# Kernel optimization log

Measured on AMD Instinct MI355X. Metric: run time of the kernel, lower is better.

Reference implementation:

```python
import jax, jax.numpy as jnp
import numpy as np

L = 15          # mp_iterations
D = 128         # node/edge feature dim
N = 50000       # n_nodes
E = 800000      # n_edges
EPS = 1e-5      # LayerNorm eps


def _mlp_ln(h, W1, b1, W2, b2, W3, b3, g, beta):
    """Linear->ReLU->Linear->ReLU->Linear->LayerNorm (torch defaults)."""
    h = jax.nn.relu(h @ W1 + b1)
    h = jax.nn.relu(h @ W2 + b2)
    h = h @ W3 + b3
    mu = h.mean(-1, keepdims=True)
    var = ((h - mu) ** 2).mean(-1, keepdims=True)
    return (h - mu) * jax.lax.rsqrt(var + EPS) * g + beta


def setup_inputs() -> dict:
    key = jax.random.key(0)
    ks = jax.random.split(key, 12)
    scale = 0.05
    x = jax.random.normal(ks[0], (N, D), dtype=jnp.float32)
    edge_index = jax.random.randint(ks[1], (2, E), 0, N, dtype=jnp.int64)
    edge_attr = jax.random.normal(ks[2], (E, D), dtype=jnp.float32)
    # Per-block stacked params (leading dim L) for edge MLP (in=3D) and node MLP (in=2D).
    inp = {
        "x": x, "edge_index": edge_index, "edge_attr": edge_attr,
        "eW1": jax.random.normal(ks[3], (L, 3 * D, D), jnp.float32) * scale,
        "eb1": jnp.zeros((L, D), jnp.float32),
        "eW2": jax.random.normal(ks[4], (L, D, D), jnp.float32) * scale,
        "eb2": jnp.zeros((L, D), jnp.float32),
        "eW3": jax.random.normal(ks[5], (L, D, D), jnp.float32) * scale,
        "eb3": jnp.zeros((L, D), jnp.float32),
        "eg": jnp.ones((L, D), jnp.float32),
        "ebeta": jnp.zeros((L, D), jnp.float32),
        "nW1": jax.random.normal(ks[6], (L, 2 * D, D), jnp.float32) * scale,
        "nb1": jnp.zeros((L, D), jnp.float32),
        "nW2": jax.random.normal(ks[7], (L, D, D), jnp.float32) * scale,
        "nb2": jnp.zeros((L, D), jnp.float32),
        "nW3": jax.random.normal(ks[8], (L, D, D), jnp.float32) * scale,
        "nb3": jnp.zeros((L, D), jnp.float32),
        "ng": jnp.ones((L, D), jnp.float32),
        "nbeta": jnp.zeros((L, D), jnp.float32),
    }
    return inp


def reference(x, edge_index, edge_attr,
              eW1, eb1, eW2, eb2, eW3, eb3, eg, ebeta,
              nW1, nb1, nW2, nb2, nW3, nb3, ng, nbeta):
    row, col = edge_index[0], edge_index[1]
    n_nodes = x.shape[0]

    params = dict(eW1=eW1, eb1=eb1, eW2=eW2, eb2=eb2, eW3=eW3, eb3=eb3,
                  eg=eg, ebeta=ebeta,
                  nW1=nW1, nb1=nb1, nW2=nW2, nb2=nb2, nW3=nW3, nb3=nb3,
                  ng=ng, nbeta=nbeta)

    def block(carry, p):
        xc, ea = carry
        # Edge update: concat(src, dest, edge_attr) -> MLP -> residual
        m = jnp.concatenate([xc[row], xc[col], ea], axis=-1)      # [E, 3D]
        ea = ea + _mlp_ln(m, p["eW1"], p["eb1"], p["eW2"], p["eb2"],
                          p["eW3"], p["eb3"], p["eg"], p["ebeta"])
        # Node update: scatter_sum over destination, concat -> MLP -> residual
        agg = jax.ops.segment_sum(ea, col, num_segments=n_nodes)  # [N, D]
        h = jnp.concatenate([xc, agg], axis=-1)                    # [N, 2D]
        xc = xc + _mlp_ln(h, p["nW1"], p["nb1"], p["nW2"], p["nb2"],
                          p["nW3"], p["nb3"], p["ng"], p["nbeta"])
        return (xc, ea), None

    (x, edge_attr), _ = jax.lax.scan(block, (x, edge_attr), params)
    return x, edge_attr
```

## Files before the change

kernel.cpp:

```cpp
#include <hip/hip_runtime.h>
#include <hip/hip_bf16.h>

#define L_ITERS 15
#define DD 128
#define NNODES 50000
#define NEDGES 800000

typedef __attribute__((ext_vector_type(4))) float f32x4;
typedef __attribute__((ext_vector_type(8))) short bf16x8;

static __device__ __forceinline__ unsigned short f2bf(float f) {
  union { float f; unsigned u; } v; v.f = f;
  unsigned r = v.u + 0x7FFFu + ((v.u >> 16) & 1u);
  return (unsigned short)(r >> 16);
}
static __device__ __forceinline__ float bf2f(unsigned short h) {
  union { unsigned u; float f; } v; v.u = (unsigned)h << 16; return v.f;
}

__global__ void pack_w_kernel(const float* __restrict__ src,
                              unsigned short* __restrict__ dst, int K) {
  int total = L_ITERS * K * DD;
  for (int i = blockIdx.x * blockDim.x + threadIdx.x; i < total;
       i += gridDim.x * blockDim.x) {
    int layer = i / (K * DD);
    int rem = i - layer * K * DD;
    int k = rem / DD, n = rem - (rem / DD) * DD;
    int s = k >> 5, hi = (k >> 3) & 3, j = k & 7;
    int t = n >> 4, lane = hi * 16 + (n & 15);
    dst[layer * K * DD + ((s * 8 + t) * 64 + lane) * 8 + j] = f2bf(src[i]);
  }
}

__global__ void cvt_kernel(const float* __restrict__ src,
                           unsigned short* __restrict__ dst,
                           int nrows, int dstride) {
  int total = nrows * 16;
  for (int p = blockIdx.x * blockDim.x + threadIdx.x; p < total;
       p += gridDim.x * blockDim.x) {
    int r = p >> 4, w = p & 15;
    const float* s = src + (long long)r * DD + w * 8;
    f32x4 a = *(const f32x4*)s, b = *(const f32x4*)(s + 4);
    bf16x8 o;
    o[0] = (short)f2bf(a[0]); o[1] = (short)f2bf(a[1]);
    o[2] = (short)f2bf(a[2]); o[3] = (short)f2bf(a[3]);
    o[4] = (short)f2bf(b[0]); o[5] = (short)f2bf(b[1]);
    o[6] = (short)f2bf(b[2]); o[7] = (short)f2bf(b[3]);
    *(bf16x8*)(dst + (long long)r * dstride + w * 8) = o;
  }
}

__global__ void hist_kernel(const int* __restrict__ ei, int* __restrict__ cnt) {
  for (int e = blockIdx.x * blockDim.x + threadIdx.x; e < NEDGES;
       e += gridDim.x * blockDim.x)
    atomicAdd(&cnt[ei[NEDGES + e]], 1);
}

__global__ __launch_bounds__(1024) void scan_kernel(const int* __restrict__ cnt,
                                                    int* __restrict__ off,
                                                    int* __restrict__ cursor) {
  __shared__ int buf[1024];
  __shared__ int base;
  if (threadIdx.x == 0) { base = 0; off[0] = 0; }
  __syncthreads();
  for (int start = 0; start < NNODES; start += 1024) {
    int i = start + threadIdx.x;
    int v = (i < NNODES) ? cnt[i] : 0;
    buf[threadIdx.x] = v;
    __syncthreads();
    for (int d = 1; d < 1024; d <<= 1) {
      int t = (threadIdx.x >= d) ? buf[threadIdx.x - d] : 0;
      __syncthreads();
      buf[threadIdx.x] += t;
      __syncthreads();
    }
    if (i < NNODES) {
      int incl = base + buf[threadIdx.x];
      off[i + 1] = incl;
      cursor[i] = incl - v;
    }
    __syncthreads();
    if (threadIdx.x == 0) base += buf[1023];
    __syncthreads();
  }
}

__global__ void scatter_kernel(const int* __restrict__ ei, int* __restrict__ cursor,
                               int* __restrict__ perm) {
  for (int e = blockIdx.x * blockDim.x + threadIdx.x; e < NEDGES;
       e += gridDim.x * blockDim.x) {
    int p = atomicAdd(&cursor[ei[NEDGES + e]], 1);
    perm[p] = e;
  }
}

template <int NS, int ROWS, int MI>
static __device__ __forceinline__ void gemm_step(
    const unsigned short* A, const unsigned short* __restrict__ pw,
    const float* __restrict__ bias, f32x4 (&acc)[MI][2],
    int lrow, int lhi, int lane, int wv, int wcol0) {
  float bv0 = bias[wcol0 + lrow];
  float bv1 = bias[wcol0 + 16 + lrow];
#pragma unroll
  for (int mi = 0; mi < MI; ++mi) {
    f32x4 z0, z1;
    z0[0] = bv0; z0[1] = bv0; z0[2] = bv0; z0[3] = bv0;
    z1[0] = bv1; z1[1] = bv1; z1[2] = bv1; z1[3] = bv1;
    acc[mi][0] = z0; acc[mi][1] = z1;
  }
  const unsigned short* bp = pw + (wv * 2 * 64 + lane) * 8;
#pragma unroll
  for (int s = 0; s < NS; ++s) {
    bf16x8 w0 = *(const bf16x8*)(bp + s * 4096);
    bf16x8 w1 = *(const bf16x8*)(bp + s * 4096 + 512);
    const unsigned short* ap = A + (s >> 2) * (ROWS * 136) + (s & 3) * 32 + lhi * 8;
#pragma unroll
    for (int mi = 0; mi < MI; ++mi) {
      bf16x8 a = *(const bf16x8*)(ap + (mi * 16 + lrow) * 136);
      acc[mi][0] = __builtin_amdgcn_mfma_f32_16x16x32_bf16(a, w0, acc[mi][0], 0, 0, 0);
      acc[mi][1] = __builtin_amdgcn_mfma_f32_16x16x32_bf16(a, w1, acc[mi][1], 0, 0, 0);
    }
  }
}

template <int MI>
static __device__ __forceinline__ void relu_store(const f32x4 (&acc)[MI][2],
                                                  unsigned short* H,
                                                  int lrow, int lhi, int wcol0) {
#pragma unroll
  for (int mi = 0; mi < MI; ++mi)
#pragma unroll
    for (int ni = 0; ni < 2; ++ni)
#pragma unroll
      for (int j = 0; j < 4; ++j)
        H[(mi * 16 + lhi * 4 + j) * 136 + wcol0 + ni * 16 + lrow] =
            f2bf(fmaxf(acc[mi][ni][j], 0.f));
}

template <bool LAST>
__global__ __launch_bounds__(256) void edge_kernel(
    const unsigned short* __restrict__ xbf, unsigned short* easlot,
    const int* __restrict__ ei,
    const unsigned short* __restrict__ pw1,
    const unsigned short* __restrict__ pw2,
    const unsigned short* __restrict__ pw3,
    const float* __restrict__ b1, const float* __restrict__ b2,
    const float* __restrict__ b3, const float* __restrict__ gg,
    const float* __restrict__ bb) {
  __shared__ unsigned short sm[3 * 64 * 136];
  __shared__ float red[128];
  constexpr int PL = 64 * 136;
  const int tid = threadIdx.x, lane = tid & 63, wv = tid >> 6;
  const int lrow = lane & 15, lhi = lane >> 4, wcol0 = wv * 32;
  const int block0 = blockIdx.x * 64;

  if (tid < 128) red[tid] = 0.f;

  {
    int r = tid >> 2, q = tid & 3;
    long long e = block0 + r;
    const unsigned short* s0 = xbf + (long long)ei[e] * DD;
    const unsigned short* s1 = xbf + (long long)ei[NEDGES + e] * DD;
    const unsigned short* s2 = easlot + e * 256;
#pragma unroll
    for (int k = 0; k < 12; ++k) {
      int w = q + 4 * k;
      int plane = w >> 4, off = (w & 15) * 8;
      const unsigned short* sp = (plane == 0) ? s0 : (plane == 1 ? s1 : s2);
      *(bf16x8*)(&sm[plane * PL + r * 136 + off]) = *(const bf16x8*)(sp + off);
    }
  }
  __syncthreads();

  f32x4 acc[4][2];
  gemm_step<12, 64, 4>(sm, pw1, b1, acc, lrow, lhi, lane, wv, wcol0);
  __syncthreads();
  relu_store<4>(acc, sm, lrow, lhi, wcol0);
  __syncthreads();
  gemm_step<4, 64, 4>(sm, pw2, b2, acc, lrow, lhi, lane, wv, wcol0);
  relu_store<4>(acc, sm + PL, lrow, lhi, wcol0);
  __syncthreads();
  gemm_step<4, 64, 4>(sm + PL, pw3, b3, acc, lrow, lhi, lane, wv, wcol0);

  float ps[4][4], pq[4][4];
#pragma unroll
  for (int mi = 0; mi < 4; ++mi)
#pragma unroll
    for (int j = 0; j < 4; ++j) {
      float a = acc[mi][0][j], b = acc[mi][1][j];
      ps[mi][j] = a + b;
      pq[mi][j] = a * a + b * b;
    }
#pragma unroll
  for (int m = 1; m < 16; m <<= 1)
#pragma unroll
    for (int mi = 0; mi < 4; ++mi)
#pragma unroll
      for (int j = 0; j < 4; ++j) {
        ps[mi][j] += __shfl_xor(ps[mi][j], m);
        pq[mi][j] += __shfl_xor(pq[mi][j], m);
      }
  if (lrow == 0)
#pragma unroll
    for (int mi = 0; mi < 4; ++mi)
#pragma unroll
      for (int j = 0; j < 4; ++j) {
        int rl = mi * 16 + lhi * 4 + j;
        atomicAdd(&red[rl * 2], ps[mi][j]);
        atomicAdd(&red[rl * 2 + 1], pq[mi][j]);
      }
  __syncthreads();

  float gv[2], bv[2];
  gv[0] = gg[wcol0 + lrow]; gv[1] = gg[wcol0 + 16 + lrow];
  bv[0] = bb[wcol0 + lrow]; bv[1] = bb[wcol0 + 16 + lrow];
  const unsigned short* P2 = sm + 2 * PL;
  float* eaf = (float*)easlot;
#pragma unroll
  for (int mi = 0; mi < 4; ++mi)
#pragma unroll
    for (int j = 0; j < 4; ++j) {
      int rl = mi * 16 + lhi * 4 + j;
      long long e = block0 + rl;
      float mu = red[rl * 2] * (1.f / DD);
      float var = red[rl * 2 + 1] * (1.f / DD) - mu * mu;
      float rstd = rsqrtf(var + 1e-5f);
#pragma unroll
      for (int ni = 0; ni < 2; ++ni) {
        int c = wcol0 + ni * 16 + lrow;
        float nv = bf2f(P2[rl * 136 + c]) +
                   (acc[mi][ni][j] - mu) * rstd * gv[ni] + bv[ni];
        if (LAST) eaf[e * 128 + c] = nv;
        else sm[rl * 136 + c] = f2bf(nv);
      }
    }
  if (!LAST) {
    __syncthreads();
#pragma unroll
    for (int p = tid; p < 1024; p += 256) {
      int r = p >> 4, off = (p & 15) * 8;
      *(bf16x8*)(easlot + (long long)(block0 + r) * 256 + off) =
          *(const bf16x8*)(sm + r * 136 + off);
    }
  }
}

template <bool LAST>
__global__ __launch_bounds__(256) void node_kernel(
    unsigned short* xbf, const unsigned short* __restrict__ easlot,
    float* xout,
    const int* __restrict__ off, const int* __restrict__ perm,
    const unsigned short* __restrict__ pw1,
    const unsigned short* __restrict__ pw2,
    const unsigned short* __restrict__ pw3,
    const float* __restrict__ b1, const float* __restrict__ b2,
    const float* __restrict__ b3, const float* __restrict__ gg,
    const float* __restrict__ bb) {
  __shared__ unsigned short sm[2 * 32 * 136];
  __shared__ float red[64];
  constexpr int PL = 32 * 136;
  const int tid = threadIdx.x, lane = tid & 63, wv = tid >> 6;
  const int lrow = lane & 15, lhi = lane >> 4, wcol0 = wv * 32;
  const int block0 = blockIdx.x * 32;

  if (tid < 64) red[tid] = 0.f;

  {
    int r = tid >> 3, c8 = tid & 7;
    int grow = block0 + r;
    int gr = grow < NNODES ? grow : NNODES - 1;
    const unsigned short* xs = xbf + (long long)gr * DD + c8 * 16;
    *(bf16x8*)(&sm[r * 136 + c8 * 16]) = *(const bf16x8*)xs;
    *(bf16x8*)(&sm[r * 136 + c8 * 16 + 8]) = *(const bf16x8*)(xs + 8);
    float a[16];
#pragma unroll
    for (int i = 0; i < 16; ++i) a[i] = 0.f;
    int p0 = off[gr], p1 = off[gr + 1];
    if (!LAST) {
      for (int p = p0; p < p1; ++p) {
        const unsigned short* ep = easlot + (long long)perm[p] * 256 + c8 * 16;
        bf16x8 u = *(const bf16x8*)ep;
        bf16x8 v = *(const bf16x8*)(ep + 8);
#pragma unroll
        for (int i = 0; i < 8; ++i) {
          a[i] += bf2f((unsigned short)u[i]);
          a[8 + i] += bf2f((unsigned short)v[i]);
        }
      }
    } else {
      const float* eaf = (const float*)easlot;
      for (int p = p0; p < p1; ++p) {
        const float* ep = eaf + (long long)perm[p] * 128 + c8 * 16;
        f32x4 u0 = *(const f32x4*)ep, u1 = *(const f32x4*)(ep + 4);
        f32x4 u2 = *(const f32x4*)(ep + 8), u3 = *(const f32x4*)(ep + 12);
#pragma unroll
        for (int i = 0; i < 4; ++i) {
          a[i] += u0[i]; a[4 + i] += u1[i]; a[8 + i] += u2[i]; a[12 + i] += u3[i];
        }
      }
    }
    bf16x8 o0, o1;
#pragma unroll
    for (int i = 0; i < 8; ++i) {
      o0[i] = (short)f2bf(a[i]);
      o1[i] = (short)f2bf(a[8 + i]);
    }
    *(bf16x8*)(&sm[PL + r * 136 + c8 * 16]) = o0;
    *(bf16x8*)(&sm[PL + r * 136 + c8 * 16 + 8]) = o1;
  }
  __syncthreads();

  f32x4 acc[2][2];
  gemm_step<8, 32, 2>(sm, pw1, b1, acc, lrow, lhi, lane, wv, wcol0);
  __syncthreads();
  relu_store<2>(acc, sm, lrow, lhi, wcol0);
  __syncthreads();
  gemm_step<4, 32, 2>(sm, pw2, b2, acc, lrow, lhi, lane, wv, wcol0);
  relu_store<2>(acc, sm + PL, lrow, lhi, wcol0);
  __syncthreads();
  gemm_step<4, 32, 2>(sm + PL, pw3, b3, acc, lrow, lhi, lane, wv, wcol0);

  float ps[2][4], pq[2][4];
#pragma unroll
  for (int mi = 0; mi < 2; ++mi)
#pragma unroll
    for (int j = 0; j < 4; ++j) {
      float a = acc[mi][0][j], b = acc[mi][1][j];
      ps[mi][j] = a + b;
      pq[mi][j] = a * a + b * b;
    }
#pragma unroll
  for (int m = 1; m < 16; m <<= 1)
#pragma unroll
    for (int mi = 0; mi < 2; ++mi)
#pragma unroll
      for (int j = 0; j < 4; ++j) {
        ps[mi][j] += __shfl_xor(ps[mi][j], m);
        pq[mi][j] += __shfl_xor(pq[mi][j], m);
      }
  if (lrow == 0)
#pragma unroll
    for (int mi = 0; mi < 2; ++mi)
#pragma unroll
      for (int j = 0; j < 4; ++j) {
        int rl = mi * 16 + lhi * 4 + j;
        atomicAdd(&red[rl * 2], ps[mi][j]);
        atomicAdd(&red[rl * 2 + 1], pq[mi][j]);
      }
  __syncthreads();

  float gv[2], bv[2];
  gv[0] = gg[wcol0 + lrow]; gv[1] = gg[wcol0 + 16 + lrow];
  bv[0] = bb[wcol0 + lrow]; bv[1] = bb[wcol0 + 16 + lrow];
#pragma unroll
  for (int mi = 0; mi < 2; ++mi)
#pragma unroll
    for (int j = 0; j < 4; ++j) {
      int rl = mi * 16 + lhi * 4 + j;
      int grow = block0 + rl;
      if (grow < NNODES) {
        float mu = red[rl * 2] * (1.f / DD);
        float var = red[rl * 2 + 1] * (1.f / DD) - mu * mu;
        float rstd = rsqrtf(var + 1e-5f);
#pragma unroll
        for (int ni = 0; ni < 2; ++ni) {
          int c = wcol0 + ni * 16 + lrow;
          float nv = bf2f(xbf[(long long)grow * DD + c]) +
                     (acc[mi][ni][j] - mu) * rstd * gv[ni] + bv[ni];
          if (LAST) xout[(long long)grow * DD + c] = nv;
          else sm[rl * 136 + c] = f2bf(nv);
        }
      }
    }
  if (!LAST) {
    __syncthreads();
#pragma unroll
    for (int p = tid; p < 512; p += 256) {
      int r = p >> 4, off2 = (p & 15) * 8;
      int grow = block0 + r;
      if (grow < NNODES)
        *(bf16x8*)(xbf + (long long)grow * DD + off2) =
            *(const bf16x8*)(sm + r * 136 + off2);
    }
  }
}

extern "C" void kernel_launch(void* const* d_in, const int* in_sizes, int n_in,
                              void* d_out, int out_size, void* d_ws, size_t ws_size,
                              hipStream_t stream) {
  const float* x  = (const float*)d_in[0];
  const int* ei   = (const int*)d_in[1];
  const float* ea = (const float*)d_in[2];
  const float* eW1 = (const float*)d_in[3];
  const float* eb1 = (const float*)d_in[4];
  const float* eW2 = (const float*)d_in[5];
  const float* eb2 = (const float*)d_in[6];
  const float* eW3 = (const float*)d_in[7];
  const float* eb3 = (const float*)d_in[8];
  const float* eg  = (const float*)d_in[9];
  const float* ebt = (const float*)d_in[10];
  const float* nW1 = (const float*)d_in[11];
  const float* nb1 = (const float*)d_in[12];
  const float* nW2 = (const float*)d_in[13];
  const float* nb2 = (const float*)d_in[14];
  const float* nW3 = (const float*)d_in[15];
  const float* nb3 = (const float*)d_in[16];
  const float* ng  = (const float*)d_in[17];
  const float* nbt = (const float*)d_in[18];

  float* xout = (float*)d_out;
  unsigned short* easlot =
      (unsigned short*)(xout + (size_t)NNODES * DD);

  unsigned short* pk_eW1 = (unsigned short*)d_ws;
  unsigned short* pk_eW2 = pk_eW1 + (size_t)L_ITERS * 384 * DD;
  unsigned short* pk_eW3 = pk_eW2 + (size_t)L_ITERS * DD * DD;
  unsigned short* pk_nW1 = pk_eW3 + (size_t)L_ITERS * DD * DD;
  unsigned short* pk_nW2 = pk_nW1 + (size_t)L_ITERS * 256 * DD;
  unsigned short* pk_nW3 = pk_nW2 + (size_t)L_ITERS * DD * DD;
  unsigned short* xbf = pk_nW3 + (size_t)L_ITERS * DD * DD;
  int* cursor = (int*)(xbf + (size_t)NNODES * DD);
  int* off    = cursor + NNODES;
  int* perm   = off + NNODES + 1;
  size_t need = (size_t)((char*)(perm + NEDGES) - (char*)d_ws);
  if (ws_size < need) return;

  pack_w_kernel<<<1024, 256, 0, stream>>>(eW1, pk_eW1, 384);
  pack_w_kernel<<<1024, 256, 0, stream>>>(eW2, pk_eW2, 128);
  pack_w_kernel<<<1024, 256, 0, stream>>>(eW3, pk_eW3, 128);
  pack_w_kernel<<<1024, 256, 0, stream>>>(nW1, pk_nW1, 256);
  pack_w_kernel<<<1024, 256, 0, stream>>>(nW2, pk_nW2, 128);
  pack_w_kernel<<<1024, 256, 0, stream>>>(nW3, pk_nW3, 128);

  cvt_kernel<<<1024, 256, 0, stream>>>(x, xbf, NNODES, 128);
  cvt_kernel<<<4096, 256, 0, stream>>>(ea, easlot, NEDGES, 256);

  hipMemsetAsync(cursor, 0, NNODES * sizeof(int), stream);
  hist_kernel<<<2048, 256, 0, stream>>>(ei, cursor);
  scan_kernel<<<1, 1024, 0, stream>>>(cursor, off, cursor);
  scatter_kernel<<<2048, 256, 0, stream>>>(ei, cursor, perm);

  for (int l = 0; l < L_ITERS; ++l) {
    if (l < L_ITERS - 1) {
      edge_kernel<false><<<NEDGES / 64, 256, 0, stream>>>(
          xbf, easlot, ei,
          pk_eW1 + (size_t)l * 384 * DD, pk_eW2 + (size_t)l * DD * DD,
          pk_eW3 + (size_t)l * DD * DD,
          eb1 + l * DD, eb2 + l * DD, eb3 + l * DD, eg + l * DD, ebt + l * DD);
      node_kernel<false><<<(NNODES + 31) / 32, 256, 0, stream>>>(
          xbf, easlot, xout, off, perm,
          pk_nW1 + (size_t)l * 256 * DD, pk_nW2 + (size_t)l * DD * DD,
          pk_nW3 + (size_t)l * DD * DD,
          nb1 + l * DD, nb2 + l * DD, nb3 + l * DD, ng + l * DD, nbt + l * DD);
    } else {
      edge_kernel<true><<<NEDGES / 64, 256, 0, stream>>>(
          xbf, easlot, ei,
          pk_eW1 + (size_t)l * 384 * DD, pk_eW2 + (size_t)l * DD * DD,
          pk_eW3 + (size_t)l * DD * DD,
          eb1 + l * DD, eb2 + l * DD, eb3 + l * DD, eg + l * DD, ebt + l * DD);
      node_kernel<true><<<(NNODES + 31) / 32, 256, 0, stream>>>(
          xbf, easlot, xout, off, perm,
          pk_nW1 + (size_t)l * 256 * DD, pk_nW2 + (size_t)l * DD * DD,
          pk_nW3 + (size_t)l * DD * DD,
          nb1 + l * DD, nb2 + l * DD, nb3 + l * DD, ng + l * DD, nbt + l * DD);
    }
  }
}
```

Before: 5.186 ms.

## Swizzle shared-memory tiles and restructure LayerNorm epilogue as row-wise vectorized pass

```diff
diff --git a/kernel.cpp b/kernel.cpp
--- a/kernel.cpp
+++ b/kernel.cpp
@@ -109,14 +109,16 @@
     acc[mi][0] = z0; acc[mi][1] = z1;
   }
   const unsigned short* bp = pw + (wv * 2 * 64 + lane) * 8;
+  const int swz = (lrow & 7) << 3;
 #pragma unroll
   for (int s = 0; s < NS; ++s) {
     bf16x8 w0 = *(const bf16x8*)(bp + s * 4096);
     bf16x8 w1 = *(const bf16x8*)(bp + s * 4096 + 512);
-    const unsigned short* ap = A + (s >> 2) * (ROWS * 136) + (s & 3) * 32 + lhi * 8;
+    const unsigned short* ap =
+        A + (s >> 2) * (ROWS * 128) + (((s & 3) * 32 + lhi * 8) ^ swz);
 #pragma unroll
     for (int mi = 0; mi < MI; ++mi) {
-      bf16x8 a = *(const bf16x8*)(ap + (mi * 16 + lrow) * 136);
+      bf16x8 a = *(const bf16x8*)(ap + (mi * 16 + lrow) * 128);
       acc[mi][0] = __builtin_amdgcn_mfma_f32_16x16x32_bf16(a, w0, acc[mi][0], 0, 0, 0);
       acc[mi][1] = __builtin_amdgcn_mfma_f32_16x16x32_bf16(a, w1, acc[mi][1], 0, 0, 0);
     }
@@ -130,11 +132,30 @@
 #pragma unroll
   for (int mi = 0; mi < MI; ++mi)
 #pragma unroll
-    for (int ni = 0; ni < 2; ++ni)
-#pragma unroll
-      for (int j = 0; j < 4; ++j)
-        H[(mi * 16 + lhi * 4 + j) * 136 + wcol0 + ni * 16 + lrow] =
+    for (int j = 0; j < 4; ++j) {
+      int row = mi * 16 + lhi * 4 + j;
+      int sw = (row & 7) << 3;
+#pragma unroll
+      for (int ni = 0; ni < 2; ++ni)
+        H[row * 128 + ((wcol0 + ni * 16 + lrow) ^ sw)] =
             f2bf(fmaxf(acc[mi][ni][j], 0.f));
+    }
+}
+
+template <int MI>
+static __device__ __forceinline__ void acc_store(const f32x4 (&acc)[MI][2],
+                                                 float* F,
+                                                 int lrow, int lhi, int wcol0) {
+#pragma unroll
+  for (int mi = 0; mi < MI; ++mi)
+#pragma unroll
+    for (int j = 0; j < 4; ++j) {
+      int row = mi * 16 + lhi * 4 + j;
+      int sw = (row & 7) << 2;
+#pragma unroll
+      for (int ni = 0; ni < 2; ++ni)
+        F[row * 128 + ((wcol0 + ni * 16 + lrow) ^ sw)] = acc[mi][ni][j];
+    }
 }
 
 template <bool LAST>
@@ -147,9 +168,9 @@
     const float* __restrict__ b1, const float* __restrict__ b2,
     const float* __restrict__ b3, const float* __restrict__ gg,
     const float* __restrict__ bb) {
-  __shared__ unsigned short sm[3 * 64 * 136];
+  constexpr int PL = 64 * 128;
+  __shared__ unsigned short sm[3 * PL];
   __shared__ float red[128];
-  constexpr int PL = 64 * 136;
   const int tid = threadIdx.x, lane = tid & 63, wv = tid >> 6;
   const int lrow = lane & 15, lhi = lane >> 4, wcol0 = wv * 32;
   const int block0 = blockIdx.x * 64;
@@ -162,12 +183,13 @@
     const unsigned short* s0 = xbf + (long long)ei[e] * DD;
     const unsigned short* s1 = xbf + (long long)ei[NEDGES + e] * DD;
     const unsigned short* s2 = easlot + e * 256;
+    const int sw = (r & 7) << 3;
 #pragma unroll
     for (int k = 0; k < 12; ++k) {
       int w = q + 4 * k;
       int plane = w >> 4, off = (w & 15) * 8;
       const unsigned short* sp = (plane == 0) ? s0 : (plane == 1 ? s1 : s2);
-      *(bf16x8*)(&sm[plane * PL + r * 136 + off]) = *(const bf16x8*)(sp + off);
+      *(bf16x8*)(&sm[plane * PL + r * 128 + (off ^ sw)]) = *(const bf16x8*)(sp + off);
     }
   }
   __syncthreads();
@@ -181,66 +203,57 @@
   relu_store<4>(acc, sm + PL, lrow, lhi, wcol0);
   __syncthreads();
   gemm_step<4, 64, 4>(sm + PL, pw3, b3, acc, lrow, lhi, lane, wv, wcol0);
-
-  float ps[4][4], pq[4][4];
-#pragma unroll
-  for (int mi = 0; mi < 4; ++mi)
-#pragma unroll
-    for (int j = 0; j < 4; ++j) {
-      float a = acc[mi][0][j], b = acc[mi][1][j];
-      ps[mi][j] = a + b;
-      pq[mi][j] = a * a + b * b;
-    }
-#pragma unroll
-  for (int m = 1; m < 16; m <<= 1)
-#pragma unroll
-    for (int mi = 0; mi < 4; ++mi)
-#pragma unroll
-      for (int j = 0; j < 4; ++j) {
-        ps[mi][j] += __shfl_xor(ps[mi][j], m);
-        pq[mi][j] += __shfl_xor(pq[mi][j], m);
-      }
-  if (lrow == 0)
-#pragma unroll
-    for (int mi = 0; mi < 4; ++mi)
-#pragma unroll
-      for (int j = 0; j < 4; ++j) {
-        int rl = mi * 16 + lhi * 4 + j;
-        atomicAdd(&red[rl * 2], ps[mi][j]);
-        atomicAdd(&red[rl * 2 + 1], pq[mi][j]);
-      }
-  __syncthreads();
-
-  float gv[2], bv[2];
-  gv[0] = gg[wcol0 + lrow]; gv[1] = gg[wcol0 + 16 + lrow];
-  bv[0] = bb[wcol0 + lrow]; bv[1] = bb[wcol0 + 16 + lrow];
+  __syncthreads();
+
+  float* F = (float*)sm;
+  acc_store<4>(acc, F, lrow, lhi, wcol0);
+  __syncthreads();
+
+  const int row = tid >> 2, cg = tid & 3;
+  const int fsw = (row & 7) << 2;
+  f32x4 av[8];
+  float s = 0.f, q2 = 0.f;
+#pragma unroll
+  for (int k = 0; k < 8; ++k) {
+    av[k] = *(const f32x4*)(F + row * 128 + ((cg * 32 + k * 4) ^ fsw));
+#pragma unroll
+    for (int i = 0; i < 4; ++i) { s += av[k][i]; q2 += av[k][i] * av[k][i]; }
+  }
+  atomicAdd(&red[row * 2], s);
+  atomicAdd(&red[row * 2 + 1], q2);
+  __syncthreads();
+
+  float mu = red[row * 2] * (1.f / DD);
+  float var = red[row * 2 + 1] * (1.f / DD) - mu * mu;
+  float rstd = rsqrtf(var + 1e-5f);
   const unsigned short* P2 = sm + 2 * PL;
+  const int ssw = (row & 7) << 3;
+  long long e = block0 + row;
   float* eaf = (float*)easlot;
 #pragma unroll
-  for (int mi = 0; mi < 4; ++mi)
-#pragma unroll
-    for (int j = 0; j < 4; ++j) {
-      int rl = mi * 16 + lhi * 4 + j;
-      long long e = block0 + rl;
-      float mu = red[rl * 2] * (1.f / DD);
-      float var = red[rl * 2 + 1] * (1.f / DD) - mu * mu;
-      float rstd = rsqrtf(var + 1e-5f);
-#pragma unroll
-      for (int ni = 0; ni < 2; ++ni) {
-        int c = wcol0 + ni * 16 + lrow;
-        float nv = bf2f(P2[rl * 136 + c]) +
-                   (acc[mi][ni][j] - mu) * rstd * gv[ni] + bv[ni];
-        if (LAST) eaf[e * 128 + c] = nv;
-        else sm[rl * 136 + c] = f2bf(nv);
-      }
-    }
-  if (!LAST) {
-    __syncthreads();
-#pragma unroll
-    for (int p = tid; p < 1024; p += 256) {
-      int r = p >> 4, off = (p & 15) * 8;
-      *(bf16x8*)(easlot + (long long)(block0 + r) * 256 + off) =
-          *(const bf16x8*)(sm + r * 136 + off);
+  for (int k = 0; k < 4; ++k) {
+    int c0 = cg * 32 + k * 8;
+    bf16x8 rv = *(const bf16x8*)(P2 + row * 128 + (c0 ^ ssw));
+    f32x4 g0 = *(const f32x4*)(gg + c0), g1 = *(const f32x4*)(gg + c0 + 4);
+    f32x4 t0 = *(const f32x4*)(bb + c0), t1 = *(const f32x4*)(bb + c0 + 4);
+    f32x4 lo = av[2 * k], hi = av[2 * k + 1];
+    float nv[8];
+#pragma unroll
+    for (int i = 0; i < 4; ++i) {
+      nv[i]     = bf2f((unsigned short)rv[i])     + (lo[i] - mu) * rstd * g0[i] + t0[i];
+      nv[4 + i] = bf2f((unsigned short)rv[4 + i]) + (hi[i] - mu) * rstd * g1[i] + t1[i];
+    }
+    if (LAST) {
+      f32x4 o0, o1;
+#pragma unroll
+      for (int i = 0; i < 4; ++i) { o0[i] = nv[i]; o1[i] = nv[4 + i]; }
+      *(f32x4*)(eaf + e * 128 + c0) = o0;
+      *(f32x4*)(eaf + e * 128 + c0 + 4) = o1;
+    } else {
+      bf16x8 o;
+#pragma unroll
+      for (int i = 0; i < 8; ++i) o[i] = (short)f2bf(nv[i]);
+      *(bf16x8*)(easlot + e * 256 + c0) = o;
     }
   }
 }
@@ -256,9 +269,10 @@
     const float* __restrict__ b1, const float* __restrict__ b2,
     const float* __restrict__ b3, const float* __restrict__ gg,
     const float* __restrict__ bb) {
-  __shared__ unsigned short sm[2 * 32 * 136];
+  constexpr int PL = 32 * 128;
+  __shared__ unsigned short sm[2 * PL];
+  __shared__ float Fbuf[32 * 128];
   __shared__ float red[64];
-  constexpr int PL = 32 * 136;
   const int tid = threadIdx.x, lane = tid & 63, wv = tid >> 6;
   const int lrow = lane & 15, lhi = lane >> 4, wcol0 = wv * 32;
   const int block0 = blockIdx.x * 32;
@@ -269,9 +283,10 @@
     int r = tid >> 3, c8 = tid & 7;
     int grow = block0 + r;
     int gr = grow < NNODES ? grow : NNODES - 1;
+    const int sw = (r & 7) << 3;
     const unsigned short* xs = xbf + (long long)gr * DD + c8 * 16;
-    *(bf16x8*)(&sm[r * 136 + c8 * 16]) = *(const bf16x8*)xs;
-    *(bf16x8*)(&sm[r * 136 + c8 * 16 + 8]) = *(const bf16x8*)(xs + 8);
+    *(bf16x8*)(&sm[r * 128 + ((c8 * 16) ^ sw)]) = *(const bf16x8*)xs;
+    *(bf16x8*)(&sm[r * 128 + ((c8 * 16 + 8) ^ sw)]) = *(const bf16x8*)(xs + 8);
     float a[16];
 #pragma unroll
     for (int i = 0; i < 16; ++i) a[i] = 0.f;
@@ -305,82 +320,70 @@
       o0[i] = (short)f2bf(a[i]);
       o1[i] = (short)f2bf(a[8 + i]);
     }
-    *(bf16x8*)(&sm[PL + r * 136 + c8 * 16]) = o0;
-    *(bf16x8*)(&sm[PL + r * 136 + c8 * 16 + 8]) = o1;
-  }
-  __syncthreads();
-
+    *(bf16x8*)(&sm[PL + r * 128 + ((c8 * 16) ^ sw)]) = o0;
+    *(bf16x8*)(&sm[PL + r * 128 + ((c8 * 16 + 8) ^ sw)]) = o1;
+  }
+  __syncthreads();
+
+  unsigned short* H1 = (unsigned short*)Fbuf;
+  unsigned short* H2 = H1 + PL;
   f32x4 acc[2][2];
   gemm_step<8, 32, 2>(sm, pw1, b1, acc, lrow, lhi, lane, wv, wcol0);
-  __syncthreads();
-  relu_store<2>(acc, sm, lrow, lhi, wcol0);
-  __syncthreads();
-  gemm_step<4, 32, 2>(sm, pw2, b2, acc, lrow, lhi, lane, wv, wcol0);
-  relu_store<2>(acc, sm + PL, lrow, lhi, wcol0);
-  __syncthreads();
-  gemm_step<4, 32, 2>(sm + PL, pw3, b3, acc, lrow, lhi, lane, wv, wcol0);
-
-  float ps[2][4], pq[2][4];
-#pragma unroll
-  for (int mi = 0; mi < 2; ++mi)
-#pragma unroll
-    for (int j = 0; j < 4; ++j) {
-      float a = acc[mi][0][j], b = acc[mi][1][j];
-      ps[mi][j] = a + b;
-      pq[mi][j] = a * a + b * b;
-    }
-#pragma unroll
-  for (int m = 1; m < 16; m <<= 1)
-#pragma unroll
-    for (int mi = 0; mi < 2; ++mi)
-#pragma unroll
-      for (int j = 0; j < 4; ++j) {
-        ps[mi][j] += __shfl_xor(ps[mi][j], m);
-        pq[mi][j] += __shfl_xor(pq[mi][j], m);
+  relu_store<2>(acc, H1, lrow, lhi, wcol0);
+  __syncthreads();
+  gemm_step<4, 32, 2>(H1, pw2, b2, acc, lrow, lhi, lane, wv, wcol0);
+  relu_store<2>(acc, H2, lrow, lhi, wcol0);
+  __syncthreads();
+  gemm_step<4, 32, 2>(H2, pw3, b3, acc, lrow, lhi, lane, wv, wcol0);
+  __syncthreads();
+  acc_store<2>(acc, Fbuf, lrow, lhi, wcol0);
+  __syncthreads();
+
+  const int row = tid >> 3, cg = tid & 7;
+  const int fsw = (row & 7) << 2;
+  f32x4 av[4];
+  float s = 0.f, q2 = 0.f;
+#pragma unroll
+  for (int k = 0; k < 4; ++k) {
+    av[k] = *(const f32x4*)(Fbuf + row * 128 + ((cg * 16 + k * 4) ^ fsw));
+#pragma unroll
+    for (int i = 0; i < 4; ++i) { s += av[k][i]; q2 += av[k][i] * av[k][i]; }
+  }
+  atomicAdd(&red[row * 2], s);
+  atomicAdd(&red[row * 2 + 1], q2);
+  __syncthreads();
+
+  int grow = block0 + row;
+  if (grow < NNODES) {
+    float mu = red[row * 2] * (1.f / DD);
+    float var = red[row * 2 + 1] * (1.f / DD) - mu * mu;
+    float rstd = rsqrtf(var + 1e-5f);
+    const int ssw = (row & 7) << 3;
+#pragma unroll
+    for (int k = 0; k < 2; ++k) {
+      int c0 = cg * 16 + k * 8;
+      bf16x8 rv = *(const bf16x8*)(sm + row * 128 + (c0 ^ ssw));
+      f32x4 g0 = *(const f32x4*)(gg + c0), g1 = *(const f32x4*)(gg + c0 + 4);
+      f32x4 t0 = *(const f32x4*)(bb + c0), t1 = *(const f32x4*)(bb + c0 + 4);
+      f32x4 lo = av[2 * k], hi = av[2 * k + 1];
+      float nv[8];
+#pragma unroll
+      for (int i = 0; i < 4; ++i) {
+        nv[i]     = bf2f((unsigned short)rv[i])     + (lo[i] - mu) * rstd * g0[i] + t0[i];
+        nv[4 + i] = bf2f((unsigned short)rv[4 + i]) + (hi[i] - mu) * rstd * g1[i] + t1[i];
       }
-  if (lrow == 0)
-#pragma unroll
-    for (int mi = 0; mi < 2; ++mi)
-#pragma unroll
-      for (int j = 0; j < 4; ++j) {
-        int rl = mi * 16 + lhi * 4 + j;
-        atomicAdd(&red[rl * 2], ps[mi][j]);
-        atomicAdd(&red[rl * 2 + 1], pq[mi][j]);
+      if (LAST) {
+        f32x4 o0, o1;
+#pragma unroll
+        for (int i = 0; i < 4; ++i) { o0[i] = nv[i]; o1[i] = nv[4 + i]; }
+        *(f32x4*)(xout + (long long)grow * DD + c0) = o0;
+        *(f32x4*)(xout + (long long)grow * DD + c0 + 4) = o1;
+      } else {
+        bf16x8 o;
+#pragma unroll
+        for (int i = 0; i < 8; ++i) o[i] = (short)f2bf(nv[i]);
+        *(bf16x8*)(xbf + (long long)grow * DD + c0) = o;
       }
-  __syncthreads();
-
-  float gv[2], bv[2];
-  gv[0] = gg[wcol0 + lrow]; gv[1] = gg[wcol0 + 16 + lrow];
-  bv[0] = bb[wcol0 + lrow]; bv[1] = bb[wcol0 + 16 + lrow];
-#pragma unroll
-  for (int mi = 0; mi < 2; ++mi)
-#pragma unroll
-    for (int j = 0; j < 4; ++j) {
-      int rl = mi * 16 + lhi * 4 + j;
-      int grow = block0 + rl;
-      if (grow < NNODES) {
-        float mu = red[rl * 2] * (1.f / DD);
-        float var = red[rl * 2 + 1] * (1.f / DD) - mu * mu;
-        float rstd = rsqrtf(var + 1e-5f);
-#pragma unroll
-        for (int ni = 0; ni < 2; ++ni) {
-          int c = wcol0 + ni * 16 + lrow;
-          float nv = bf2f(xbf[(long long)grow * DD + c]) +
-                     (acc[mi][ni][j] - mu) * rstd * gv[ni] + bv[ni];
-          if (LAST) xout[(long long)grow * DD + c] = nv;
-          else sm[rl * 136 + c] = f2bf(nv);
-        }
-      }
-    }
-  if (!LAST) {
-    __syncthreads();
-#pragma unroll
-    for (int p = tid; p < 512; p += 256) {
-      int r = p >> 4, off2 = (p & 15) * 8;
-      int grow = block0 + r;
-      if (grow < NNODES)
-        *(bf16x8*)(xbf + (long long)grow * DD + off2) =
-            *(const bf16x8*)(sm + r * 136 + off2);
     }
   }
 }
```

New measurement: 6.493 ms. +25.2%, slower.

## Shrink edge kernel LDS by reading edge_attr operand directly from global

Applied to the files above, without the earlier changes.

```diff
diff --git a/kernel.cpp b/kernel.cpp
--- a/kernel.cpp
+++ b/kernel.cpp
@@ -138,7 +138,7 @@
 }
 
 template <bool LAST>
-__global__ __launch_bounds__(256) void edge_kernel(
+__global__ __launch_bounds__(256, 4) void edge_kernel(
     const unsigned short* __restrict__ xbf, unsigned short* easlot,
     const int* __restrict__ ei,
     const unsigned short* __restrict__ pw1,
@@ -147,9 +147,9 @@
     const float* __restrict__ b1, const float* __restrict__ b2,
     const float* __restrict__ b3, const float* __restrict__ gg,
     const float* __restrict__ bb) {
-  __shared__ unsigned short sm[3 * 64 * 136];
+  constexpr int PL = 64 * 136;
+  __shared__ unsigned short sm[2 * PL];
   __shared__ float red[128];
-  constexpr int PL = 64 * 136;
   const int tid = threadIdx.x, lane = tid & 63, wv = tid >> 6;
   const int lrow = lane & 15, lhi = lane >> 4, wcol0 = wv * 32;
   const int block0 = blockIdx.x * 64;
@@ -161,19 +161,45 @@
     long long e = block0 + r;
     const unsigned short* s0 = xbf + (long long)ei[e] * DD;
     const unsigned short* s1 = xbf + (long long)ei[NEDGES + e] * DD;
-    const unsigned short* s2 = easlot + e * 256;
-#pragma unroll
-    for (int k = 0; k < 12; ++k) {
+#pragma unroll
+    for (int k = 0; k < 8; ++k) {
       int w = q + 4 * k;
       int plane = w >> 4, off = (w & 15) * 8;
-      const unsigned short* sp = (plane == 0) ? s0 : (plane == 1 ? s1 : s2);
+      const unsigned short* sp = (plane == 0) ? s0 : s1;
       *(bf16x8*)(&sm[plane * PL + r * 136 + off]) = *(const bf16x8*)(sp + off);
     }
   }
   __syncthreads();
 
   f32x4 acc[4][2];
-  gemm_step<12, 64, 4>(sm, pw1, b1, acc, lrow, lhi, lane, wv, wcol0);
+  {
+    float bv0 = b1[wcol0 + lrow], bv1 = b1[wcol0 + 16 + lrow];
+#pragma unroll
+    for (int mi = 0; mi < 4; ++mi) {
+      f32x4 z0, z1;
+      z0[0] = bv0; z0[1] = bv0; z0[2] = bv0; z0[3] = bv0;
+      z1[0] = bv1; z1[1] = bv1; z1[2] = bv1; z1[3] = bv1;
+      acc[mi][0] = z0; acc[mi][1] = z1;
+    }
+    const unsigned short* bp = pw1 + (wv * 2 * 64 + lane) * 8;
+#pragma unroll
+    for (int s = 0; s < 12; ++s) {
+      bf16x8 w0 = *(const bf16x8*)(bp + s * 4096);
+      bf16x8 w1 = *(const bf16x8*)(bp + s * 4096 + 512);
+#pragma unroll
+      for (int mi = 0; mi < 4; ++mi) {
+        bf16x8 a;
+        if (s < 8)
+          a = *(const bf16x8*)(sm + (s >> 2) * PL + (mi * 16 + lrow) * 136 +
+                               (s & 3) * 32 + lhi * 8);
+        else
+          a = *(const bf16x8*)(easlot + (long long)(block0 + mi * 16 + lrow) * 256 +
+                               (s - 8) * 32 + lhi * 8);
+        acc[mi][0] = __builtin_amdgcn_mfma_f32_16x16x32_bf16(a, w0, acc[mi][0], 0, 0, 0);
+        acc[mi][1] = __builtin_amdgcn_mfma_f32_16x16x32_bf16(a, w1, acc[mi][1], 0, 0, 0);
+      }
+    }
+  }
   __syncthreads();
   relu_store<4>(acc, sm, lrow, lhi, wcol0);
   __syncthreads();
@@ -214,8 +240,7 @@
   float gv[2], bv[2];
   gv[0] = gg[wcol0 + lrow]; gv[1] = gg[wcol0 + 16 + lrow];
   bv[0] = bb[wcol0 + lrow]; bv[1] = bb[wcol0 + 16 + lrow];
-  const unsigned short* P2 = sm + 2 * PL;
-  float* eaf = (float*)easlot;
+  float* F = (float*)sm;
 #pragma unroll
   for (int mi = 0; mi < 4; ++mi)
 #pragma unroll
@@ -228,19 +253,27 @@
 #pragma unroll
       for (int ni = 0; ni < 2; ++ni) {
         int c = wcol0 + ni * 16 + lrow;
-        float nv = bf2f(P2[rl * 136 + c]) +
+        float nv = bf2f(easlot[e * 256 + c]) +
                    (acc[mi][ni][j] - mu) * rstd * gv[ni] + bv[ni];
-        if (LAST) eaf[e * 128 + c] = nv;
+        if (LAST) F[rl * 128 + c] = nv;
         else sm[rl * 136 + c] = f2bf(nv);
       }
     }
-  if (!LAST) {
-    __syncthreads();
+  __syncthreads();
+  if (LAST) {
+    float* eaf = (float*)easlot;
+#pragma unroll
+    for (int p = tid; p < 2048; p += 256) {
+      int r = p >> 5, o = (p & 31) * 4;
+      *(f32x4*)(eaf + (long long)(block0 + r) * 128 + o) =
+          *(const f32x4*)(F + r * 128 + o);
+    }
+  } else {
 #pragma unroll
     for (int p = tid; p < 1024; p += 256) {
-      int r = p >> 4, off = (p & 15) * 8;
-      *(bf16x8*)(easlot + (long long)(block0 + r) * 256 + off) =
-          *(const bf16x8*)(sm + r * 136 + off);
+      int r = p >> 4, o = (p & 15) * 8;
+      *(bf16x8*)(easlot + (long long)(block0 + r) * 256 + o) =
+          *(const bf16x8*)(sm + r * 136 + o);
     }
   }
 }
```

Measured after the change: 6.359 ms. 1.23x slower.

## Give each wave its own 16-edge tile in edge MLP kernel, dropping block barriers

Applied to the files above, without the earlier changes.

```diff
diff --git a/kernel.cpp b/kernel.cpp
--- a/kernel.cpp
+++ b/kernel.cpp
@@ -138,7 +138,7 @@
 }
 
 template <bool LAST>
-__global__ __launch_bounds__(256) void edge_kernel(
+__global__ __launch_bounds__(256, 3) void edge_kernel(
     const unsigned short* __restrict__ xbf, unsigned short* easlot,
     const int* __restrict__ ei,
     const unsigned short* __restrict__ pw1,
@@ -147,100 +147,159 @@
     const float* __restrict__ b1, const float* __restrict__ b2,
     const float* __restrict__ b3, const float* __restrict__ gg,
     const float* __restrict__ bb) {
-  __shared__ unsigned short sm[3 * 64 * 136];
-  __shared__ float red[128];
-  constexpr int PL = 64 * 136;
+  __shared__ unsigned short sm[4 * 16 * 384];
   const int tid = threadIdx.x, lane = tid & 63, wv = tid >> 6;
-  const int lrow = lane & 15, lhi = lane >> 4, wcol0 = wv * 32;
-  const int block0 = blockIdx.x * 64;
-
-  if (tid < 128) red[tid] = 0.f;
+  const int lrow = lane & 15, lhi = lane >> 4;
+  unsigned short* R = sm + wv * (16 * 384);
+  const long long block0 = (long long)blockIdx.x * 64 + wv * 16;
 
   {
-    int r = tid >> 2, q = tid & 3;
+    int r = lane >> 2, q = lane & 3;
     long long e = block0 + r;
     const unsigned short* s0 = xbf + (long long)ei[e] * DD;
     const unsigned short* s1 = xbf + (long long)ei[NEDGES + e] * DD;
     const unsigned short* s2 = easlot + e * 256;
+    const int swz = (r & 7) << 3;
 #pragma unroll
     for (int k = 0; k < 12; ++k) {
       int w = q + 4 * k;
       int plane = w >> 4, off = (w & 15) * 8;
-      const unsigned short* sp = (plane == 0) ? s0 : (plane == 1 ? s1 : s2);
-      *(bf16x8*)(&sm[plane * PL + r * 136 + off]) = *(const bf16x8*)(sp + off);
-    }
-  }
-  __syncthreads();
-
-  f32x4 acc[4][2];
-  gemm_step<12, 64, 4>(sm, pw1, b1, acc, lrow, lhi, lane, wv, wcol0);
-  __syncthreads();
-  relu_store<4>(acc, sm, lrow, lhi, wcol0);
-  __syncthreads();
-  gemm_step<4, 64, 4>(sm, pw2, b2, acc, lrow, lhi, lane, wv, wcol0);
-  relu_store<4>(acc, sm + PL, lrow, lhi, wcol0);
-  __syncthreads();
-  gemm_step<4, 64, 4>(sm + PL, pw3, b3, acc, lrow, lhi, lane, wv, wcol0);
-
-  float ps[4][4], pq[4][4];
-#pragma unroll
-  for (int mi = 0; mi < 4; ++mi)
-#pragma unroll
-    for (int j = 0; j < 4; ++j) {
-      float a = acc[mi][0][j], b = acc[mi][1][j];
-      ps[mi][j] = a + b;
-      pq[mi][j] = a * a + b * b;
-    }
-#pragma unroll
-  for (int m = 1; m < 16; m <<= 1)
-#pragma unroll
-    for (int mi = 0; mi < 4; ++mi)
-#pragma unroll
-      for (int j = 0; j < 4; ++j) {
-        ps[mi][j] += __shfl_xor(ps[mi][j], m);
-        pq[mi][j] += __shfl_xor(pq[mi][j], m);
-      }
-  if (lrow == 0)
-#pragma unroll
-    for (int mi = 0; mi < 4; ++mi)
-#pragma unroll
-      for (int j = 0; j < 4; ++j) {
-        int rl = mi * 16 + lhi * 4 + j;
-        atomicAdd(&red[rl * 2], ps[mi][j]);
-        atomicAdd(&red[rl * 2 + 1], pq[mi][j]);
-      }
-  __syncthreads();
-
-  float gv[2], bv[2];
-  gv[0] = gg[wcol0 + lrow]; gv[1] = gg[wcol0 + 16 + lrow];
-  bv[0] = bb[wcol0 + lrow]; bv[1] = bb[wcol0 + 16 + lrow];
-  const unsigned short* P2 = sm + 2 * PL;
-  float* eaf = (float*)easlot;
-#pragma unroll
-  for (int mi = 0; mi < 4; ++mi)
-#pragma unroll
-    for (int j = 0; j < 4; ++j) {
-      int rl = mi * 16 + lhi * 4 + j;
-      long long e = block0 + rl;
-      float mu = red[rl * 2] * (1.f / DD);
-      float var = red[rl * 2 + 1] * (1.f / DD) - mu * mu;
-      float rstd = rsqrtf(var + 1e-5f);
-#pragma unroll
-      for (int ni = 0; ni < 2; ++ni) {
-        int c = wcol0 + ni * 16 + lrow;
-        float nv = bf2f(P2[rl * 136 + c]) +
-                   (acc[mi][ni][j] - mu) * rstd * gv[ni] + bv[ni];
-        if (LAST) eaf[e * 128 + c] = nv;
-        else sm[rl * 136 + c] = f2bf(nv);
-      }
-    }
-  if (!LAST) {
-    __syncthreads();
-#pragma unroll
-    for (int p = tid; p < 1024; p += 256) {
-      int r = p >> 4, off = (p & 15) * 8;
-      *(bf16x8*)(easlot + (long long)(block0 + r) * 256 + off) =
-          *(const bf16x8*)(sm + r * 136 + off);
+      const unsigned short* sp = plane == 0 ? s0 : (plane == 1 ? s1 : s2);
+      *(bf16x8*)(&R[r * 384 + plane * 128 + (off ^ swz)]) =
+          *(const bf16x8*)(sp + off);
+    }
+  }
+
+  const int aswz = (lrow & 7) << 3;
+  f32x4 acc[8];
+
+  {
+#pragma unroll
+    for (int t = 0; t < 8; ++t) {
+      float bv = b1[t * 16 + lrow];
+      f32x4 z; z[0] = bv; z[1] = bv; z[2] = bv; z[3] = bv;
+      acc[t] = z;
+    }
+#pragma unroll
+    for (int s = 0; s < 12; ++s) {
+      bf16x8 a = *(const bf16x8*)(
+          &R[lrow * 384 + (s >> 2) * 128 + ((((s & 3) * 32) + lhi * 8) ^ aswz)]);
+#pragma unroll
+      for (int t = 0; t < 8; ++t) {
+        bf16x8 w = *(const bf16x8*)(pw1 + ((s * 8 + t) * 64 + lane) * 8);
+        acc[t] = __builtin_amdgcn_mfma_f32_16x16x32_bf16(a, w, acc[t], 0, 0, 0);
+      }
+    }
+  }
+#pragma unroll
+  for (int j = 0; j < 4; ++j) {
+    int row = lhi * 4 + j;
+    int swz = (row & 7) << 3;
+#pragma unroll
+    for (int t = 0; t < 8; ++t)
+      R[row * 384 + ((t * 16 + lrow) ^ swz)] = f2bf(fmaxf(acc[t][j], 0.f));
+  }
+
+  {
+#pragma unroll
+    for (int t = 0; t < 8; ++t) {
+      float bv = b2[t * 16 + lrow];
+      f32x4 z; z[0] = bv; z[1] = bv; z[2] = bv; z[3] = bv;
+      acc[t] = z;
+    }
+#pragma unroll
+    for (int s = 0; s < 4; ++s) {
+      bf16x8 a = *(const bf16x8*)(&R[lrow * 384 + ((s * 32 + lhi * 8) ^ aswz)]);
+#pragma unroll
+      for (int t = 0; t < 8; ++t) {
+        bf16x8 w = *(const bf16x8*)(pw2 + ((s * 8 + t) * 64 + lane) * 8);
+        acc[t] = __builtin_amdgcn_mfma_f32_16x16x32_bf16(a, w, acc[t], 0, 0, 0);
+      }
+    }
+  }
+#pragma unroll
+  for (int j = 0; j < 4; ++j) {
+    int row = lhi * 4 + j;
+    int swz = (row & 7) << 3;
+#pragma unroll
+    for (int t = 0; t < 8; ++t)
+      R[row * 384 + 128 + ((t * 16 + lrow) ^ swz)] = f2bf(fmaxf(acc[t][j], 0.f));
+  }
+
+  {
+#pragma unroll
+    for (int t = 0; t < 8; ++t) {
+      float bv = b3[t * 16 + lrow];
+      f32x4 z; z[0] = bv; z[1] = bv; z[2] = bv; z[3] = bv;
+      acc[t] = z;
+    }
+#pragma unroll
+    for (int s = 0; s < 4; ++s) {
+      bf16x8 a = *(const bf16x8*)(
+          &R[lrow * 384 + 128 + ((s * 32 + lhi * 8) ^ aswz)]);
+#pragma unroll
+      for (int t = 0; t < 8; ++t) {
+        bf16x8 w = *(const bf16x8*)(pw3 + ((s * 8 + t) * 64 + lane) * 8);
+        acc[t] = __builtin_amdgcn_mfma_f32_16x16x32_bf16(a, w, acc[t], 0, 0, 0);
+      }
+    }
+  }
+
+  float mu[4], rstd[4];
+#pragma unroll
+  for (int j = 0; j < 4; ++j) {
+    float s = 0.f, q2 = 0.f;
+#pragma unroll
+    for (int t = 0; t < 8; ++t) { float v = acc[t][j]; s += v; q2 += v * v; }
+#pragma unroll
+    for (int m = 1; m < 16; m <<= 1) {
+      s += __shfl_xor(s, m);
+      q2 += __shfl_xor(q2, m);
+    }
+    mu[j] = s * (1.f / DD);
+    float var = q2 * (1.f / DD) - mu[j] * mu[j];
+    rstd[j] = rsqrtf(var + 1e-5f);
+  }
+
+  float gv[8], tv[8];
+#pragma unroll
+  for (int t = 0; t < 8; ++t) {
+    gv[t] = gg[t * 16 + lrow];
+    tv[t] = bb[t * 16 + lrow];
+  }
+  float* Fw = (float*)R;
+#pragma unroll
+  for (int j = 0; j < 4; ++j) {
+    int row = lhi * 4 + j;
+    int swz = (row & 7) << 3;
+    int fswz = (row & 7) << 2;
+#pragma unroll
+    for (int t = 0; t < 8; ++t) {
+      int c = t * 16 + lrow;
+      float nv = bf2f(R[row * 384 + 256 + (c ^ swz)]) +
+                 (acc[t][j] - mu[j]) * rstd[j] * gv[t] + tv[t];
+      if (LAST) Fw[row * 192 + (c ^ fswz)] = nv;
+      else R[row * 384 + (c ^ swz)] = f2bf(nv);
+    }
+  }
+
+  if (LAST) {
+    float* eaf = (float*)easlot;
+    const float* F = (const float*)R;
+#pragma unroll
+    for (int k = 0; k < 8; ++k) {
+      int p = lane + 64 * k;
+      int row = p >> 5, o = (p & 31) * 4;
+      *(f32x4*)(eaf + (block0 + row) * 128 + o) =
+          *(const f32x4*)(F + row * 192 + (o ^ ((row & 7) << 2)));
+    }
+  } else {
+#pragma unroll
+    for (int k = 0; k < 4; ++k) {
+      int p = lane + 64 * k;
+      int row = p >> 4, o = (p & 15) * 8;
+      *(bf16x8*)(easlot + (block0 + row) * 256 + o) =
+          *(const bf16x8*)(&R[row * 384 + (o ^ ((row & 7) << 3))]);
     }
   }
 }
```

After: 8.264 ms. +59.4%, slower.
